# Kernel optimization log

Hardware: AMD Instinct MI355X
Metric: run time of the kernel (lower is better)

Reference implementation:

```python
import jax, jax.numpy as jnp
import numpy as np

B, NB, H, C = 32, 1024, 768, 64


def setup_inputs() -> dict:
    key = jax.random.key(0)
    k1, k2, k3, k4, k5, k6 = jax.random.split(key, 6)
    block_tokens = jax.random.normal(k1, (B, NB, H), dtype=jnp.float32)
    block_active = jax.random.randint(k2, (B, NB), 0, 2) == 1
    block_to_channel_map = jax.random.randint(k3, (NB,), 0, C, dtype=jnp.int64)
    # agg_gate params: Linear(H, H//2) -> Tanh -> Linear(H//2, 1)
    s1 = 1.0 / np.sqrt(H)
    s2 = 1.0 / np.sqrt(H // 2)
    W1 = jax.random.uniform(k4, (H, H // 2), jnp.float32, -s1, s1)
    b1 = jnp.zeros((H // 2,), jnp.float32)
    W2 = jax.random.uniform(k5, (H // 2, 1), jnp.float32, -s2, s2)
    b2 = jnp.zeros((1,), jnp.float32)
    return {"block_tokens": block_tokens, "block_active": block_active,
            "block_to_channel_map": block_to_channel_map,
            "W1": W1, "b1": b1, "W2": W2, "b2": b2}


def reference(block_tokens, block_active, block_to_channel_map, W1, b1, W2, b2):
    # gate MLP: (B, NB)
    h = jnp.tanh(jnp.einsum('bnh,hk->bnk', block_tokens, W1) + b1)
    gate = (jnp.einsum('bnk,ko->bno', h, W2) + b2).squeeze(-1)  # (B, NB)

    # (C, NB) one-hot channel membership; (B, C, NB) active-per-channel mask
    onehot = block_to_channel_map[None, :] == jnp.arange(C)[:, None]
    mask = block_active[:, None, :] & onehot[None, :, :]  # (B, C, NB)

    neg_inf = jnp.float32(-jnp.inf)
    g = jnp.where(mask, gate[:, None, :], neg_inf)  # (B, C, NB)
    m = jnp.max(g, axis=-1, keepdims=True)
    m_safe = jnp.where(jnp.isfinite(m), m, 0.0)  # guard all-masked channels
    e = jnp.where(mask, jnp.exp(g - m_safe), 0.0)
    s = jnp.sum(e, axis=-1, keepdims=True)
    w = jnp.where(s > 0, e / jnp.where(s > 0, s, 1.0), 0.0)  # softmax, nan->0

    channel_tokens = jnp.einsum('bcn,bnh->bch', w, block_tokens)  # (B, C, H)
    channel_active = jnp.any(mask, axis=-1)  # (B, C)
    return channel_tokens, channel_active
```

## Files before the change

kernel.cpp:

```cpp
#include <hip/hip_runtime.h>
#include <math.h>

#define B_    32
#define NB_   1024
#define H_    768
#define K_    384
#define C_    64
#define ROWS_ 32
#define NSTEP_ 24

typedef __attribute__((ext_vector_type(8))) short bf16x8;
typedef __attribute__((ext_vector_type(4))) float f32x4;

__device__ __forceinline__ short f2bf(float f) {
    unsigned u = __float_as_uint(f);
    unsigned r = (u + 0x7fffu + ((u >> 16) & 1u)) >> 16;
    return (short)r;
}
__device__ __forceinline__ float ftanh(float x) {
    float e = __expf(2.f * x);
    return 1.f - 2.f * __builtin_amdgcn_rcpf(e + 1.f);
}

__global__ __launch_bounds__(256) void prep_w1(const float* __restrict__ W1,
                                               short* __restrict__ swz)
{
    int idx = blockIdx.x * 256 + threadIdx.x;
    int k = idx / K_, n = idx % K_;
    float v = W1[idx];
    int s = k >> 5, g = (k >> 3) & 3, i = k & 7;
    int t = n >> 4, nn = n & 15;
    swz[((s * 24 + t) * 512) + (g * 16 + nn) * 8 + i] = f2bf(v);
}

__global__ __launch_bounds__(1024) void compact_kernel(
    const int* __restrict__ active, int* __restrict__ list, int* __restrict__ cnt)
{
    __shared__ int wsum[16];
    __shared__ int wbase[17];
    const int b = blockIdx.x, tid = threadIdx.x, lane = tid & 63, wid = tid >> 6;
    const int flag = active[b * NB_ + tid] != 0;
    const unsigned long long m = __ballot(flag);
    if (lane == 0) wsum[wid] = __popcll(m);
    __syncthreads();
    if (tid == 0) {
        int r = 0;
        for (int i = 0; i < 16; ++i) { wbase[i] = r; r += wsum[i]; }
        wbase[16] = r;
        cnt[b] = r;
    }
    __syncthreads();
    const int total = wbase[16];
    if (flag) {
        const int pos = wbase[wid] + __popcll(m & ((1ull << lane) - 1ull));
        list[b * NB_ + pos] = tid;
    }
    if (tid >= total) list[b * NB_ + tid] = 0;
}

__global__ __launch_bounds__(256, 2) void gate_kernel(
    const float* __restrict__ tokens, const short* __restrict__ swz,
    const float* __restrict__ b1, const float* __restrict__ W2,
    const float* __restrict__ b2, const int* __restrict__ list,
    const int* __restrict__ cnt, float* __restrict__ gate)
{
    __shared__ __align__(16) short As[2][1024];
    __shared__ float red[4][32];

    const int b = blockIdx.x >> 5;
    const int chunk = blockIdx.x & 31;
    if (chunk * ROWS_ >= cnt[b]) return;

    const int tid = threadIdx.x;
    const int lane = tid & 63;
    const int w = tid >> 6;

    const int r   = tid >> 3;
    const int c8  = tid & 7;
    const int g2w = c8 >> 1, hw = c8 & 1;
    const int fw  = r >> 4,  roww = r & 15;
    const int woff = ((fw * 4 + g2w) * 16 + (roww ^ (g2w << 1))) * 8 + hw * 4;
    const int nrow = list[b * NB_ + chunk * ROWS_ + r];
    const float* aptr = tokens + ((size_t)b * NB_ + nrow) * H_ + c8 * 4;

    const int g2r  = lane >> 4;
    const int rowr = (lane & 15) ^ (g2r << 1);
    const int roff0 = ((0 + g2r) * 16 + rowr) * 8;
    const int roff1 = ((4 + g2r) * 16 + rowr) * 8;

    const short* bbase = swz + (w * 6) * 512 + lane * 8;

    f32x4 acc[6][2];
#pragma unroll
    for (int j = 0; j < 6; ++j)
#pragma unroll
        for (int f = 0; f < 2; ++f) acc[j][f] = (f32x4){0.f, 0.f, 0.f, 0.f};

    float4 pa[4];
    bf16x8 bs[3][6];

    pa[0] = *(const float4*)(aptr + 0 * 32);
    pa[1] = *(const float4*)(aptr + 1 * 32);
    pa[2] = *(const float4*)(aptr + 2 * 32);
    pa[3] = *(const float4*)(aptr + 3 * 32);
#pragma unroll
    for (int j = 0; j < 6; ++j)
        bs[0][j] = *(const bf16x8*)(bbase + 0 * 12288 + j * 512);
#pragma unroll
    for (int j = 0; j < 6; ++j)
        bs[1][j] = *(const bf16x8*)(bbase + 1 * 12288 + j * 512);
    {
        short4 av = {f2bf(pa[0].x), f2bf(pa[0].y), f2bf(pa[0].z), f2bf(pa[0].w)};
        *(short4*)&As[0][woff] = av;
    }
    asm volatile("s_waitcnt lgkmcnt(0)" ::: "memory");
    __builtin_amdgcn_s_barrier();
    __builtin_amdgcn_sched_barrier(0);

#pragma unroll
    for (int s = 0; s < NSTEP_; ++s) {
        if (s + 4 < NSTEP_)
            pa[(s + 4) & 3] = *(const float4*)(aptr + (s + 4) * 32);
        if (s + 2 < NSTEP_) {
            const short* bp = bbase + (size_t)(s + 2) * 12288;
#pragma unroll
            for (int j = 0; j < 6; ++j)
                bs[(s + 2) % 3][j] = *(const bf16x8*)(bp + j * 512);
        }
        {
            bf16x8 a0 = *(const bf16x8*)&As[s & 1][roff0];
            bf16x8 a1 = *(const bf16x8*)&As[s & 1][roff1];
#pragma unroll
            for (int j = 0; j < 6; ++j) {
                acc[j][0] = __builtin_amdgcn_mfma_f32_16x16x32_bf16(
                                a0, bs[s % 3][j], acc[j][0], 0, 0, 0);
                acc[j][1] = __builtin_amdgcn_mfma_f32_16x16x32_bf16(
                                a1, bs[s % 3][j], acc[j][1], 0, 0, 0);
            }
        }
        if (s + 1 < NSTEP_) {
            float4 q = pa[(s + 1) & 3];
            short4 av = {f2bf(q.x), f2bf(q.y), f2bf(q.z), f2bf(q.w)};
            *(short4*)&As[(s + 1) & 1][woff] = av;
        }
        asm volatile("s_waitcnt lgkmcnt(0)" ::: "memory");
        __builtin_amdgcn_s_barrier();
        __builtin_amdgcn_sched_barrier(0);
    }

    float ps[2][4];
#pragma unroll
    for (int f = 0; f < 2; ++f)
#pragma unroll
        for (int rr = 0; rr < 4; ++rr) ps[f][rr] = 0.f;

#pragma unroll
    for (int j = 0; j < 6; ++j) {
        const int n = (w * 6 + j) * 16 + (lane & 15);
        const float bb = b1[n];
        const float ww = W2[n];
#pragma unroll
        for (int f = 0; f < 2; ++f)
#pragma unroll
            for (int rr = 0; rr < 4; ++rr)
                ps[f][rr] += ftanh(acc[j][f][rr] + bb) * ww;
    }
#pragma unroll
    for (int m = 1; m < 16; m <<= 1)
#pragma unroll
        for (int f = 0; f < 2; ++f)
#pragma unroll
            for (int rr = 0; rr < 4; ++rr)
                ps[f][rr] += __shfl_xor(ps[f][rr], m, 64);

    if ((lane & 15) == 0) {
        const int rbase = (lane >> 4) * 4;
#pragma unroll
        for (int f = 0; f < 2; ++f)
#pragma unroll
            for (int rr = 0; rr < 4; ++rr)
                red[w][f * 16 + rbase + rr] = ps[f][rr];
    }
    __syncthreads();
    if (tid < ROWS_) {
        float sg = b2[0];
#pragma unroll
        for (int q = 0; q < 4; ++q) sg += red[q][tid];
        gate[b * NB_ + list[b * NB_ + chunk * ROWS_ + tid]] = sg;
    }
}

__global__ __launch_bounds__(256) void agg_kernel(
    const float* __restrict__ tokens, const int* __restrict__ active,
    const int* __restrict__ cmap, const float* __restrict__ gate,
    float* __restrict__ out_tok, float* __restrict__ out_act)
{
    __shared__ float wls[NB_];
    __shared__ float red[256];
    __shared__ int   idxs[NB_];
    __shared__ float wts[NB_];
    __shared__ int   gbase[17];

    const int b = blockIdx.x >> 6, c = blockIdx.x & 63;
    const int tid = threadIdx.x, lane = tid & 63, wid = tid >> 6;

    float lmax = -INFINITY;
    for (int n = tid; n < NB_; n += 256) {
        const bool msk = (active[b * NB_ + n] != 0) && (cmap[n] == c);
        const float g  = msk ? gate[b * NB_ + n] : -INFINITY;
        wls[n] = g;
        lmax = fmaxf(lmax, g);
    }
    red[tid] = lmax; __syncthreads();
    for (int s = 128; s > 0; s >>= 1) {
        if (tid < s) red[tid] = fmaxf(red[tid], red[tid + s]);
        __syncthreads();
    }
    const float m = red[0]; __syncthreads();
    const float msafe = (m > -INFINITY) ? m : 0.f;

    float lsum = 0.f;
    for (int n = tid; n < NB_; n += 256) {
        const float g = wls[n];
        const float e = (g > -INFINITY) ? __expf(g - msafe) : 0.f;
        wls[n] = e; lsum += e;
    }
    red[tid] = lsum; __syncthreads();
    for (int s = 128; s > 0; s >>= 1) {
        if (tid < s) red[tid] += red[tid + s];
        __syncthreads();
    }
    const float ssum = red[0];
    const float inv  = (ssum > 0.f) ? 1.f / ssum : 0.f;
    __syncthreads();

#pragma unroll
    for (int it = 0; it < 4; ++it) {
        const int n = it * 256 + wid * 64 + lane;
        const unsigned long long mask = __ballot(wls[n] > 0.f);
        if (lane == 0) gbase[1 + it * 4 + wid] = __popcll(mask);
    }
    __syncthreads();
    if (tid == 0) {
        gbase[0] = 0;
        for (int i = 1; i <= 16; ++i) gbase[i] += gbase[i - 1];
    }
    __syncthreads();
#pragma unroll
    for (int it = 0; it < 4; ++it) {
        const int n = it * 256 + wid * 64 + lane;
        const float e = wls[n];
        const unsigned long long mask = __ballot(e > 0.f);
        if (e > 0.f) {
            const int pos = gbase[it * 4 + wid] +
                            __popcll(mask & ((1ull << lane) - 1ull));
            idxs[pos] = n;
            wts[pos]  = e * inv;
        }
    }
    __syncthreads();
    const int cnt = gbase[16];

    if (tid < 192) {
        const int d = tid * 4;
        const float* tb = tokens + (size_t)b * NB_ * H_ + d;
        float4 a = {0.f, 0.f, 0.f, 0.f};
        for (int i = 0; i < cnt; ++i) {
            const float wv = wts[i];
            const float4 v = *(const float4*)(tb + (size_t)idxs[i] * H_);
            a.x += wv * v.x; a.y += wv * v.y;
            a.z += wv * v.z; a.w += wv * v.w;
        }
        *(float4*)(out_tok + ((size_t)(b * C_ + c)) * H_ + d) = a;
    }
    if (tid == 0) out_act[b * C_ + c] = (m > -INFINITY) ? 1.f : 0.f;
}

extern "C" void kernel_launch(void* const* d_in, const int* in_sizes, int n_in,
                              void* d_out, int out_size, void* d_ws, size_t ws_size,
                              hipStream_t stream)
{
    const float* tokens = (const float*)d_in[0];
    const int*   active = (const int*)  d_in[1];
    const int*   cmap   = (const int*)  d_in[2];
    const float* W1     = (const float*)d_in[3];
    const float* b1     = (const float*)d_in[4];
    const float* W2     = (const float*)d_in[5];
    const float* b2     = (const float*)d_in[6];

    float* out      = (float*)d_out;
    float* out_act  = out + (size_t)B_ * C_ * H_;

    short* swz     = (short*)d_ws;
    float* gate_ws = (float*)((char*)d_ws + 589824);
    int*   list    = (int*)  ((char*)d_ws + 720896);
    int*   cntb    = (int*)  ((char*)d_ws + 851968);

    compact_kernel<<<B_, 1024, 0, stream>>>(active, list, cntb);
    prep_w1<<<(H_ * K_) / 256, 256, 0, stream>>>(W1, swz);
    gate_kernel<<<B_ * 32, 256, 0, stream>>>(tokens, swz, b1, W2, b2, list, cntb, gate_ws);
    agg_kernel<<<B_ * C_, 256, 0, stream>>>(tokens, active, cmap, gate_ws, out, out_act);
}
```

Baseline: 57.54 us.

## Stage full A tile into LDS upfront and drop per-step barriers in gate GEMM

The gate kernel now loads and converts the whole 32x768 token tile into shared memory (48 KB) in four batches of six loads before the MFMA loop. It then runs all 24 K-steps without any per-step barrier or double-buffer handoff. This removes 24 workgroup syncs and lets many global loads be in flight at once. In exchange, LDS use per block grows a lot and occupancy is bounded by shared memory. The launch-bounds hint is raised to 3 blocks per CU, which also tightens the register budget.

```diff
diff --git a/kernel.cpp b/kernel.cpp
--- a/kernel.cpp
+++ b/kernel.cpp
@@ -58,13 +58,13 @@
     if (tid >= total) list[b * NB_ + tid] = 0;
 }
 
-__global__ __launch_bounds__(256, 2) void gate_kernel(
+__global__ __launch_bounds__(256, 3) void gate_kernel(
     const float* __restrict__ tokens, const short* __restrict__ swz,
     const float* __restrict__ b1, const float* __restrict__ W2,
     const float* __restrict__ b2, const int* __restrict__ list,
     const int* __restrict__ cnt, float* __restrict__ gate)
 {
-    __shared__ __align__(16) short As[2][1024];
+    __shared__ __align__(16) short As[NSTEP_ * 1024];
     __shared__ float red[4][32];
 
     const int b = blockIdx.x >> 5;
@@ -90,62 +90,52 @@
 
     const short* bbase = swz + (w * 6) * 512 + lane * 8;
 
-    f32x4 acc[6][2];
-#pragma unroll
-    for (int j = 0; j < 6; ++j)
-#pragma unroll
-        for (int f = 0; f < 2; ++f) acc[j][f] = (f32x4){0.f, 0.f, 0.f, 0.f};
-
-    float4 pa[4];
     bf16x8 bs[3][6];
-
-    pa[0] = *(const float4*)(aptr + 0 * 32);
-    pa[1] = *(const float4*)(aptr + 1 * 32);
-    pa[2] = *(const float4*)(aptr + 2 * 32);
-    pa[3] = *(const float4*)(aptr + 3 * 32);
 #pragma unroll
     for (int j = 0; j < 6; ++j)
         bs[0][j] = *(const bf16x8*)(bbase + 0 * 12288 + j * 512);
 #pragma unroll
     for (int j = 0; j < 6; ++j)
         bs[1][j] = *(const bf16x8*)(bbase + 1 * 12288 + j * 512);
-    {
-        short4 av = {f2bf(pa[0].x), f2bf(pa[0].y), f2bf(pa[0].z), f2bf(pa[0].w)};
-        *(short4*)&As[0][woff] = av;
-    }
-    asm volatile("s_waitcnt lgkmcnt(0)" ::: "memory");
-    __builtin_amdgcn_s_barrier();
-    __builtin_amdgcn_sched_barrier(0);
+
+#pragma unroll
+    for (int g = 0; g < 4; ++g) {
+        float4 pa[6];
+#pragma unroll
+        for (int q = 0; q < 6; ++q)
+            pa[q] = *(const float4*)(aptr + (g * 6 + q) * 32);
+#pragma unroll
+        for (int q = 0; q < 6; ++q) {
+            short4 av = {f2bf(pa[q].x), f2bf(pa[q].y), f2bf(pa[q].z), f2bf(pa[q].w)};
+            *(short4*)&As[(g * 6 + q) * 1024 + woff] = av;
+        }
+    }
+
+    f32x4 acc[6][2];
+#pragma unroll
+    for (int j = 0; j < 6; ++j)
+#pragma unroll
+        for (int f = 0; f < 2; ++f) acc[j][f] = (f32x4){0.f, 0.f, 0.f, 0.f};
+
+    __syncthreads();
 
 #pragma unroll
     for (int s = 0; s < NSTEP_; ++s) {
-        if (s + 4 < NSTEP_)
-            pa[(s + 4) & 3] = *(const float4*)(aptr + (s + 4) * 32);
         if (s + 2 < NSTEP_) {
             const short* bp = bbase + (size_t)(s + 2) * 12288;
 #pragma unroll
             for (int j = 0; j < 6; ++j)
                 bs[(s + 2) % 3][j] = *(const bf16x8*)(bp + j * 512);
         }
-        {
-            bf16x8 a0 = *(const bf16x8*)&As[s & 1][roff0];
-            bf16x8 a1 = *(const bf16x8*)&As[s & 1][roff1];
-#pragma unroll
-            for (int j = 0; j < 6; ++j) {
-                acc[j][0] = __builtin_amdgcn_mfma_f32_16x16x32_bf16(
-                                a0, bs[s % 3][j], acc[j][0], 0, 0, 0);
-                acc[j][1] = __builtin_amdgcn_mfma_f32_16x16x32_bf16(
-                                a1, bs[s % 3][j], acc[j][1], 0, 0, 0);
-            }
-        }
-        if (s + 1 < NSTEP_) {
-            float4 q = pa[(s + 1) & 3];
-            short4 av = {f2bf(q.x), f2bf(q.y), f2bf(q.z), f2bf(q.w)};
-            *(short4*)&As[(s + 1) & 1][woff] = av;
-        }
-        asm volatile("s_waitcnt lgkmcnt(0)" ::: "memory");
-        __builtin_amdgcn_s_barrier();
-        __builtin_amdgcn_sched_barrier(0);
+        bf16x8 a0 = *(const bf16x8*)&As[s * 1024 + roff0];
+        bf16x8 a1 = *(const bf16x8*)&As[s * 1024 + roff1];
+#pragma unroll
+        for (int j = 0; j < 6; ++j) {
+            acc[j][0] = __builtin_amdgcn_mfma_f32_16x16x32_bf16(
+                            a0, bs[s % 3][j], acc[j][0], 0, 0, 0);
+            acc[j][1] = __builtin_amdgcn_mfma_f32_16x16x32_bf16(
+                            a1, bs[s % 3][j], acc[j][1], 0, 0, 0);
+        }
     }
 
     float ps[2][4];
```

Result: slower. 63.16 us (+9.8%).
